# Kernel optimization log

Hardware: AMD Instinct MI355X
Metric: run time of the kernel (lower is better)

Reference implementation:

```python
import jax, jax.numpy as jnp
import numpy as np

MARGIN = 0.3
PD_EPS = 1e-6  # torch.nn.functional.pairwise_distance default eps (added to the diff)


def setup_inputs() -> dict:
    key = jax.random.key(0)
    k1, k2 = jax.random.split(key)
    n, d = 8192, 128
    inputs = jax.random.normal(k1, (n, d), dtype=jnp.float32)
    positive = jax.random.normal(k2, (n, d), dtype=jnp.float32)
    return {"inputs": inputs, "positive": positive}


def reference(inputs, positive):
    # Pairwise squared Euclidean distances: ||xi||^2 + ||xj||^2 - 2 xi.xj  -> [n, n]
    sq = jnp.sum(inputs * inputs, axis=1, keepdims=True)  # [n, 1]
    dist = sq + sq.T - 2.0 * (inputs @ inputs.T)
    dist = jnp.sqrt(jnp.clip(dist, 1e-12, None))

    # Original: dist[i].argsort()[4] -> 5th-nearest (index 0 is self at ~0 distance).
    # Equivalent, avoiding full per-row sort: top-5 smallest distances.
    _, idx = jax.lax.top_k(-dist, 5)  # idx: [n, 5], ascending by distance
    negative = inputs[idx[:, 4]]  # hard negatives, [n, d]

    # TripletMarginLoss(margin=0.3, p=2): pairwise_distance adds eps to the diff.
    d_ap = jnp.linalg.norm(inputs - positive + PD_EPS, axis=1)
    d_an = jnp.linalg.norm(inputs - negative + PD_EPS, axis=1)
    return jnp.mean(jnp.maximum(d_ap - d_an + MARGIN, 0.0))
```

## Files before the change

kernel.cpp:

```cpp
#include <hip/hip_runtime.h>

#define NN 8192
#define DD 128
#define CH 16
#define CPC (NN / CH)
#define TILES (CPC / 64)
#define NPART 64

typedef __bf16 bf16x8 __attribute__((ext_vector_type(8)));
typedef float f32x4 __attribute__((ext_vector_type(4)));

#define PACK_INIT __uint_as_float(0x7F7FFFFFu)

static __device__ __forceinline__ float packsi(float s, unsigned idx) {
  return __uint_as_float((__float_as_uint(s) & 0xFFFFE000u) | idx);
}

#define NET4(S0, S1, S2, S3, v)                                                \
  {                                                                            \
    float v_ = (v), o0 = S0, o1 = S1, o2 = S2;                                 \
    S0 = fminf(o0, v_);                                                        \
    S1 = __builtin_amdgcn_fmed3f(v_, o0, o1);                                  \
    S2 = __builtin_amdgcn_fmed3f(v_, o1, o2);                                  \
    S3 = __builtin_amdgcn_fmed3f(v_, o2, S3);                                  \
  }
#define NET5(S0, S1, S2, S3, S4, v)                                            \
  {                                                                            \
    float v_ = (v), o0 = S0, o1 = S1, o2 = S2, o3 = S3;                        \
    S0 = fminf(o0, v_);                                                        \
    S1 = __builtin_amdgcn_fmed3f(v_, o0, o1);                                  \
    S2 = __builtin_amdgcn_fmed3f(v_, o1, o2);                                  \
    S3 = __builtin_amdgcn_fmed3f(v_, o2, o3);                                  \
    S4 = __builtin_amdgcn_fmed3f(v_, o3, S4);                                  \
  }

static __device__ __forceinline__ unsigned short f2bf(float f) {
  unsigned u = __float_as_uint(f);
  u += 0x7FFFu + ((u >> 16) & 1u);
  return (unsigned short)(u >> 16);
}

__global__ __launch_bounds__(256) void prep_kernel(const float* __restrict__ x,
                                                   unsigned short* __restrict__ xb,
                                                   float* __restrict__ sq,
                                                   float* __restrict__ partial) {
  const int wave = threadIdx.x >> 6, lane = threadIdx.x & 63;
  const int row = blockIdx.x * 4 + wave;
  const float2 v = ((const float2*)(x + (size_t)row * DD))[lane];
  float ss = v.x * v.x + v.y * v.y;
#pragma unroll
  for (int off = 32; off; off >>= 1) ss += __shfl_down(ss, off);
  if (lane == 0) sq[row] = ss;
  unsigned packed = (unsigned)f2bf(v.x) | ((unsigned)f2bf(v.y) << 16);
  ((unsigned*)(xb + (size_t)row * DD))[lane] = packed;
  if (blockIdx.x == 0 && threadIdx.x < NPART) partial[threadIdx.x] = 0.0f;
}

__global__ __launch_bounds__(256, 2) void dist_topk_kernel(
    const unsigned short* __restrict__ xb, const float* __restrict__ sq,
    float* __restrict__ pscore) {
  const int t = threadIdx.x;
  const int wave = t >> 6, lane = t & 63;
  const int lrow = lane & 15, lquad = lane >> 4;
  const int rowBase = blockIdx.x * 256;
  const int chunk = blockIdx.y;
  const int j0 = chunk * CPC;
  const bool hasDiag = ((blockIdx.x >> 1) == (int)blockIdx.y);

  __shared__ unsigned short colsB[2][64 * DD];
  __shared__ float sqs[2][64];

  const int r0 = rowBase + wave * 64 + lrow;
  const unsigned short* ap0 = xb + (size_t)(r0)*DD + lquad * 8;
  const unsigned short* ap1 = xb + (size_t)(r0 + 16) * DD + lquad * 8;
  const unsigned short* ap2 = xb + (size_t)(r0 + 32) * DD + lquad * 8;
  const unsigned short* ap3 = xb + (size_t)(r0 + 48) * DD + lquad * 8;
  bf16x8 a00 = *(const bf16x8*)(ap0), a01 = *(const bf16x8*)(ap0 + 32),
         a02 = *(const bf16x8*)(ap0 + 64), a03 = *(const bf16x8*)(ap0 + 96);
  bf16x8 a10 = *(const bf16x8*)(ap1), a11 = *(const bf16x8*)(ap1 + 32),
         a12 = *(const bf16x8*)(ap1 + 64), a13 = *(const bf16x8*)(ap1 + 96);
  bf16x8 a20 = *(const bf16x8*)(ap2), a21 = *(const bf16x8*)(ap2 + 32),
         a22 = *(const bf16x8*)(ap2 + 64), a23 = *(const bf16x8*)(ap2 + 96);
  bf16x8 a30 = *(const bf16x8*)(ap3), a31 = *(const bf16x8*)(ap3 + 32),
         a32 = *(const bf16x8*)(ap3 + 64), a33 = *(const bf16x8*)(ap3 + 96);

  float q00 = PACK_INIT, q01 = PACK_INIT, q02 = PACK_INIT, q03 = PACK_INIT,
        q04 = PACK_INIT;
  float q10 = PACK_INIT, q11 = PACK_INIT, q12 = PACK_INIT, q13 = PACK_INIT,
        q14 = PACK_INIT;
  float q20 = PACK_INIT, q21 = PACK_INIT, q22 = PACK_INIT, q23 = PACK_INIT,
        q24 = PACK_INIT;
  float q30 = PACK_INIT, q31 = PACK_INIT, q32 = PACK_INIT, q33 = PACK_INIT,
        q34 = PACK_INIT;

  const int sr = t >> 4, sch = t & 15;
  const int dst0 = (sr << 4) | (sch ^ (sr & 15));

  const float4* srcv = (const float4*)(xb + (size_t)j0 * DD);
  float4 g0 = srcv[t], g1 = srcv[t + 256], g2 = srcv[t + 512], g3 = srcv[t + 768];
  float sqv = 0.0f;
  if (t < 64) sqv = sq[j0 + t];

#define KBODY(INSROW)                                                          \
  for (int it = 0; it < TILES; ++it) {                                         \
    const int jt = j0 + it * 64;                                               \
    const int cur = it & 1;                                                    \
    {                                                                          \
      float4* dstv = (float4*)colsB[cur];                                      \
      dstv[dst0] = g0;                                                         \
      dstv[dst0 + 256] = g1;                                                   \
      dstv[dst0 + 512] = g2;                                                   \
      dstv[dst0 + 768] = g3;                                                   \
      if (t < 64) sqs[cur][t] = sqv;                                           \
    }                                                                          \
    if (it + 1 < TILES) {                                                      \
      const float4* nsrc = (const float4*)(xb + (size_t)(jt + 64) * DD);       \
      g0 = nsrc[t]; g1 = nsrc[t + 256]; g2 = nsrc[t + 512]; g3 = nsrc[t + 768];\
      if (t < 64) sqv = sq[jt + 64 + t];                                       \
    }                                                                          \
    __syncthreads();                                                           \
    _Pragma("unroll")                                                          \
    for (int ct = 0; ct < 4; ++ct) {                                           \
      const unsigned short* bb = &colsB[cur][(ct * 16 + lrow) * DD];           \
      bf16x8 b0 = *(const bf16x8*)(bb + (((0 + lquad) ^ lrow) << 3));          \
      bf16x8 b1 = *(const bf16x8*)(bb + (((4 + lquad) ^ lrow) << 3));          \
      bf16x8 b2 = *(const bf16x8*)(bb + (((8 + lquad) ^ lrow) << 3));          \
      bf16x8 b3 = *(const bf16x8*)(bb + (((12 + lquad) ^ lrow) << 3));         \
      f32x4 ac0 = {0.f, 0.f, 0.f, 0.f}, ac1 = {0.f, 0.f, 0.f, 0.f};           \
      f32x4 ac2 = {0.f, 0.f, 0.f, 0.f}, ac3 = {0.f, 0.f, 0.f, 0.f};           \
      ac0 = __builtin_amdgcn_mfma_f32_16x16x32_bf16(b0, a00, ac0, 0, 0, 0);    \
      ac1 = __builtin_amdgcn_mfma_f32_16x16x32_bf16(b0, a10, ac1, 0, 0, 0);    \
      ac2 = __builtin_amdgcn_mfma_f32_16x16x32_bf16(b0, a20, ac2, 0, 0, 0);    \
      ac3 = __builtin_amdgcn_mfma_f32_16x16x32_bf16(b0, a30, ac3, 0, 0, 0);    \
      ac0 = __builtin_amdgcn_mfma_f32_16x16x32_bf16(b1, a01, ac0, 0, 0, 0);    \
      ac1 = __builtin_amdgcn_mfma_f32_16x16x32_bf16(b1, a11, ac1, 0, 0, 0);    \
      ac2 = __builtin_amdgcn_mfma_f32_16x16x32_bf16(b1, a21, ac2, 0, 0, 0);    \
      ac3 = __builtin_amdgcn_mfma_f32_16x16x32_bf16(b1, a31, ac3, 0, 0, 0);    \
      ac0 = __builtin_amdgcn_mfma_f32_16x16x32_bf16(b2, a02, ac0, 0, 0, 0);    \
      ac1 = __builtin_amdgcn_mfma_f32_16x16x32_bf16(b2, a12, ac1, 0, 0, 0);    \
      ac2 = __builtin_amdgcn_mfma_f32_16x16x32_bf16(b2, a22, ac2, 0, 0, 0);    \
      ac3 = __builtin_amdgcn_mfma_f32_16x16x32_bf16(b2, a32, ac3, 0, 0, 0);    \
      ac0 = __builtin_amdgcn_mfma_f32_16x16x32_bf16(b3, a03, ac0, 0, 0, 0);    \
      ac1 = __builtin_amdgcn_mfma_f32_16x16x32_bf16(b3, a13, ac1, 0, 0, 0);    \
      ac2 = __builtin_amdgcn_mfma_f32_16x16x32_bf16(b3, a23, ac2, 0, 0, 0);    \
      ac3 = __builtin_amdgcn_mfma_f32_16x16x32_bf16(b3, a33, ac3, 0, 0, 0);    \
      const f32x4 sq4 = *(const f32x4*)&sqs[cur][ct * 16 + lquad * 4];         \
      const unsigned colb = (unsigned)(jt + ct * 16 + lquad * 4);              \
      _Pragma("unroll")                                                        \
      for (int r = 0; r < 4; ++r) {                                            \
        INSROW(0, packsi(fmaf(-2.0f, ac0[r], sq4[r]), colb + r));              \
        INSROW(1, packsi(fmaf(-2.0f, ac1[r], sq4[r]), colb + r));              \
        INSROW(2, packsi(fmaf(-2.0f, ac2[r], sq4[r]), colb + r));              \
        INSROW(3, packsi(fmaf(-2.0f, ac3[r], sq4[r]), colb + r));              \
      }                                                                        \
    }                                                                          \
  }

#define INS4(G, V) NET4(q##G##0, q##G##1, q##G##2, q##G##3, (V))
#define INS5(G, V) NET5(q##G##0, q##G##1, q##G##2, q##G##3, q##G##4, (V))

  if (hasDiag) {
    KBODY(INS5)
  } else {
    KBODY(INS4)
  }
#undef KBODY

#define MERGE4(G, M)                                                           \
  {                                                                            \
    float o0 = __shfl_xor(q##G##0, M), o1 = __shfl_xor(q##G##1, M),            \
          o2 = __shfl_xor(q##G##2, M), o3 = __shfl_xor(q##G##3, M);            \
    NET4(q##G##0, q##G##1, q##G##2, q##G##3, o0);                              \
    NET4(q##G##0, q##G##1, q##G##2, q##G##3, o1);                              \
    NET4(q##G##0, q##G##1, q##G##2, q##G##3, o2);                              \
    NET4(q##G##0, q##G##1, q##G##2, q##G##3, o3);                              \
  }
#define MERGE5(G, M)                                                           \
  {                                                                            \
    float o0 = __shfl_xor(q##G##0, M), o1 = __shfl_xor(q##G##1, M),            \
          o2 = __shfl_xor(q##G##2, M), o3 = __shfl_xor(q##G##3, M),            \
          o4 = __shfl_xor(q##G##4, M);                                         \
    NET5(q##G##0, q##G##1, q##G##2, q##G##3, q##G##4, o0);                     \
    NET5(q##G##0, q##G##1, q##G##2, q##G##3, q##G##4, o1);                     \
    NET5(q##G##0, q##G##1, q##G##2, q##G##3, q##G##4, o2);                     \
    NET5(q##G##0, q##G##1, q##G##2, q##G##3, q##G##4, o3);                     \
    NET5(q##G##0, q##G##1, q##G##2, q##G##3, q##G##4, o4);                     \
  }
  if (hasDiag) {
    MERGE5(0, 16) MERGE5(1, 16) MERGE5(2, 16) MERGE5(3, 16)
    MERGE5(0, 32) MERGE5(1, 32) MERGE5(2, 32) MERGE5(3, 32)
  } else {
    MERGE4(0, 16) MERGE4(1, 16) MERGE4(2, 16) MERGE4(3, 16)
    MERGE4(0, 32) MERGE4(1, 32) MERGE4(2, 32) MERGE4(3, 32)
  }

  if (lquad == 0) {
    float* b0p = pscore + (size_t)(r0)*80 + chunk * 5;
    b0p[0] = q00; b0p[1] = q01; b0p[2] = q02; b0p[3] = q03; b0p[4] = q04;
    float* b1p = pscore + (size_t)(r0 + 16) * 80 + chunk * 5;
    b1p[0] = q10; b1p[1] = q11; b1p[2] = q12; b1p[3] = q13; b1p[4] = q14;
    float* b2p = pscore + (size_t)(r0 + 32) * 80 + chunk * 5;
    b2p[0] = q20; b2p[1] = q21; b2p[2] = q22; b2p[3] = q23; b2p[4] = q24;
    float* b3p = pscore + (size_t)(r0 + 48) * 80 + chunk * 5;
    b3p[0] = q30; b3p[1] = q31; b3p[2] = q32; b3p[3] = q33; b3p[4] = q34;
  }
}

__global__ __launch_bounds__(256) void final_kernel(const float* __restrict__ x,
                                                    const float* __restrict__ pos,
                                                    const float* __restrict__ pscore,
                                                    float* __restrict__ partial) {
  const int wave = threadIdx.x >> 6, lane = threadIdx.x & 63;
  const int row = blockIdx.x * 4 + wave;

  float q0 = PACK_INIT, q1 = PACK_INIT, q2 = PACK_INIT, q3 = PACK_INIT,
        q4 = PACK_INIT;
  if (lane < CH) {
    const float* b = pscore + (size_t)row * 80 + lane * 5;
    q0 = b[0]; q1 = b[1]; q2 = b[2]; q3 = b[3]; q4 = b[4];
  }
#pragma unroll
  for (int m = 1; m < CH; m <<= 1) {
    float o0 = __shfl_xor(q0, m), o1 = __shfl_xor(q1, m), o2 = __shfl_xor(q2, m),
          o3 = __shfl_xor(q3, m), o4 = __shfl_xor(q4, m);
    NET5(q0, q1, q2, q3, q4, o0);
    NET5(q0, q1, q2, q3, q4, o1);
    NET5(q0, q1, q2, q3, q4, o2);
    NET5(q0, q1, q2, q3, q4, o3);
    NET5(q0, q1, q2, q3, q4, o4);
  }
  const int nidx = (int)(__float_as_uint(__shfl(q4, 0)) & 0x1FFFu);

  const float2 xv  = ((const float2*)(x   + (size_t)row  * DD))[lane];
  const float2 pv  = ((const float2*)(pos + (size_t)row  * DD))[lane];
  const float2 nvv = ((const float2*)(x   + (size_t)nidx * DD))[lane];
  float a0 = xv.x - pv.x + 1e-6f, a1 = xv.y - pv.y + 1e-6f;
  float b0 = xv.x - nvv.x + 1e-6f, b1 = xv.y - nvv.y + 1e-6f;
  float dap = a0 * a0 + a1 * a1;
  float dan = b0 * b0 + b1 * b1;
#pragma unroll
  for (int off = 32; off; off >>= 1) {
    dap += __shfl_down(dap, off);
    dan += __shfl_down(dan, off);
  }
  __shared__ float hs[4];
  if (lane == 0) hs[wave] = fmaxf(sqrtf(dap) - sqrtf(dan) + 0.3f, 0.0f);
  __syncthreads();
  if (threadIdx.x == 0) {
    float s = hs[0] + hs[1] + hs[2] + hs[3];
    atomicAdd(&partial[blockIdx.x & (NPART - 1)], s);
  }
}

__global__ __launch_bounds__(64) void reduce_kernel(const float* __restrict__ partial,
                                                    float* __restrict__ out) {
  float v = partial[threadIdx.x];
#pragma unroll
  for (int off = 32; off; off >>= 1) v += __shfl_down(v, off);
  if (threadIdx.x == 0) out[0] = v * (1.0f / 8192.0f);
}

extern "C" void kernel_launch(void* const* d_in, const int* in_sizes, int n_in,
                              void* d_out, int out_size, void* d_ws, size_t ws_size,
                              hipStream_t stream) {
  const float* x   = (const float*)d_in[0];
  const float* pos = (const float*)d_in[1];
  float* out = (float*)d_out;

  char* w = (char*)d_ws;
  unsigned short* xb = (unsigned short*)w;
  float* sq = (float*)(w + (size_t)NN * DD * 2);
  float* pscore = (float*)(w + (size_t)NN * DD * 2 + (size_t)NN * 4);
  float* partial = (float*)(w + (size_t)NN * DD * 2 + (size_t)NN * 4 +
                            (size_t)NN * 80 * 4);

  prep_kernel<<<NN / 4, 256, 0, stream>>>(x, xb, sq, partial);
  dist_topk_kernel<<<dim3(NN / 256, CH), 256, 0, stream>>>(xb, sq, pscore);
  final_kernel<<<NN / 4, 256, 0, stream>>>(x, pos, pscore, partial);
  reduce_kernel<<<1, 64, 0, stream>>>(partial, out);
}
```

Measured before the change: 109.0 us.

## Fold norm into MFMA accumulator init and stream column tiles via global_load_lds

The per-column norm term is precomputed as -0.5*||x||^2 - 70 and fed in as the MFMA accumulator's initial value. This removes the per-element fmaf from the top-k insertion loop, and the selection flips to a max-network on negated scores. Column tiles are now loaded straight into LDS with global_load_lds instead of passing through registers, and all column norms are staged up front. This cuts VGPR pressure and per-element ALU work. The risk is that the -70 offset, which keeps scores negative so the packed index bits order correctly, may affect precision, and only the single barrier at loop top remains for async-load ordering.

```diff
diff --git a/kernel.cpp b/kernel.cpp
--- a/kernel.cpp
+++ b/kernel.cpp
@@ -10,7 +10,7 @@
 typedef __bf16 bf16x8 __attribute__((ext_vector_type(8)));
 typedef float f32x4 __attribute__((ext_vector_type(4)));
 
-#define PACK_INIT __uint_as_float(0x7F7FFFFFu)
+#define PACK_INIT __uint_as_float(0xFF7FFFFFu)
 
 static __device__ __forceinline__ float packsi(float s, unsigned idx) {
   return __uint_as_float((__float_as_uint(s) & 0xFFFFE000u) | idx);
@@ -19,7 +19,7 @@
 #define NET4(S0, S1, S2, S3, v)                                                \
   {                                                                            \
     float v_ = (v), o0 = S0, o1 = S1, o2 = S2;                                 \
-    S0 = fminf(o0, v_);                                                        \
+    S0 = fmaxf(o0, v_);                                                        \
     S1 = __builtin_amdgcn_fmed3f(v_, o0, o1);                                  \
     S2 = __builtin_amdgcn_fmed3f(v_, o1, o2);                                  \
     S3 = __builtin_amdgcn_fmed3f(v_, o2, S3);                                  \
@@ -27,7 +27,7 @@
 #define NET5(S0, S1, S2, S3, S4, v)                                            \
   {                                                                            \
     float v_ = (v), o0 = S0, o1 = S1, o2 = S2, o3 = S3;                        \
-    S0 = fminf(o0, v_);                                                        \
+    S0 = fmaxf(o0, v_);                                                        \
     S1 = __builtin_amdgcn_fmed3f(v_, o0, o1);                                  \
     S2 = __builtin_amdgcn_fmed3f(v_, o1, o2);                                  \
     S3 = __builtin_amdgcn_fmed3f(v_, o2, o3);                                  \
@@ -38,6 +38,12 @@
   unsigned u = __float_as_uint(f);
   u += 0x7FFFu + ((u >> 16) & 1u);
   return (unsigned short)(u >> 16);
+}
+
+static __device__ __forceinline__ void gload_lds16(const void* g, void* l) {
+  __builtin_amdgcn_global_load_lds(
+      (const __attribute__((address_space(1))) unsigned*)g,
+      (__attribute__((address_space(3))) unsigned*)l, 16, 0, 0);
 }
 
 __global__ __launch_bounds__(256) void prep_kernel(const float* __restrict__ x,
@@ -50,7 +56,7 @@
   float ss = v.x * v.x + v.y * v.y;
 #pragma unroll
   for (int off = 32; off; off >>= 1) ss += __shfl_down(ss, off);
-  if (lane == 0) sq[row] = ss;
+  if (lane == 0) sq[row] = fmaf(-0.5f, ss, -70.0f);
   unsigned packed = (unsigned)f2bf(v.x) | ((unsigned)f2bf(v.y) << 16);
   ((unsigned*)(xb + (size_t)row * DD))[lane] = packed;
   if (blockIdx.x == 0 && threadIdx.x < NPART) partial[threadIdx.x] = 0.0f;
@@ -68,7 +74,7 @@
   const bool hasDiag = ((blockIdx.x >> 1) == (int)blockIdx.y);
 
   __shared__ unsigned short colsB[2][64 * DD];
-  __shared__ float sqs[2][64];
+  __shared__ float sqs_all[CPC];
 
   const int r0 = rowBase + wave * 64 + lrow;
   const unsigned short* ap0 = xb + (size_t)(r0)*DD + lquad * 8;
@@ -93,32 +99,28 @@
   float q30 = PACK_INIT, q31 = PACK_INIT, q32 = PACK_INIT, q33 = PACK_INIT,
         q34 = PACK_INIT;
 
-  const int sr = t >> 4, sch = t & 15;
-  const int dst0 = (sr << 4) | (sch ^ (sr & 15));
-
-  const float4* srcv = (const float4*)(xb + (size_t)j0 * DD);
-  float4 g0 = srcv[t], g1 = srcv[t + 256], g2 = srcv[t + 512], g3 = srcv[t + 768];
-  float sqv = 0.0f;
-  if (t < 64) sqv = sq[j0 + t];
+  const int psl = (t & ~15) | ((t ^ (t >> 4)) & 15);
+
+#define ISSUE_TILE(buf, jtrow)                                                 \
+  {                                                                            \
+    const float4* s_ = (const float4*)(xb + (size_t)(jtrow)*DD);               \
+    char* l_ = (char*)(&colsB[buf][0]) + wave * 1024;                          \
+    gload_lds16(s_ + psl, l_);                                                 \
+    gload_lds16(s_ + psl + 256, l_ + 4096);                                    \
+    gload_lds16(s_ + psl + 512, l_ + 8192);                                    \
+    gload_lds16(s_ + psl + 768, l_ + 12288);                                   \
+  }
+
+  sqs_all[t] = sq[j0 + t];
+  sqs_all[t + 256] = sq[j0 + 256 + t];
+  ISSUE_TILE(0, j0)
 
 #define KBODY(INSROW)                                                          \
   for (int it = 0; it < TILES; ++it) {                                         \
     const int jt = j0 + it * 64;                                               \
     const int cur = it & 1;                                                    \
-    {                                                                          \
-      float4* dstv = (float4*)colsB[cur];                                      \
-      dstv[dst0] = g0;                                                         \
-      dstv[dst0 + 256] = g1;                                                   \
-      dstv[dst0 + 512] = g2;                                                   \
-      dstv[dst0 + 768] = g3;                                                   \
-      if (t < 64) sqs[cur][t] = sqv;                                           \
-    }                                                                          \
-    if (it + 1 < TILES) {                                                      \
-      const float4* nsrc = (const float4*)(xb + (size_t)(jt + 64) * DD);       \
-      g0 = nsrc[t]; g1 = nsrc[t + 256]; g2 = nsrc[t + 512]; g3 = nsrc[t + 768];\
-      if (t < 64) sqv = sq[jt + 64 + t];                                       \
-    }                                                                          \
-    __syncthreads();                                                           \
+    __syncthreads();          \
+    if (it + 1 < TILES) { ISSUE_TILE(cur ^ 1, jt + 64) }                       \
     _Pragma("unroll")                                                          \
     for (int ct = 0; ct < 4; ++ct) {                                           \
       const unsigned short* bb = &colsB[cur][(ct * 16 + lrow) * DD];           \
@@ -126,12 +128,11 @@
       bf16x8 b1 = *(const bf16x8*)(bb + (((4 + lquad) ^ lrow) << 3));          \
       bf16x8 b2 = *(const bf16x8*)(bb + (((8 + lquad) ^ lrow) << 3));          \
       bf16x8 b3 = *(const bf16x8*)(bb + (((12 + lquad) ^ lrow) << 3));         \
-      f32x4 ac0 = {0.f, 0.f, 0.f, 0.f}, ac1 = {0.f, 0.f, 0.f, 0.f};           \
-      f32x4 ac2 = {0.f, 0.f, 0.f, 0.f}, ac3 = {0.f, 0.f, 0.f, 0.f};           \
-      ac0 = __builtin_amdgcn_mfma_f32_16x16x32_bf16(b0, a00, ac0, 0, 0, 0);    \
-      ac1 = __builtin_amdgcn_mfma_f32_16x16x32_bf16(b0, a10, ac1, 0, 0, 0);    \
-      ac2 = __builtin_amdgcn_mfma_f32_16x16x32_bf16(b0, a20, ac2, 0, 0, 0);    \
-      ac3 = __builtin_amdgcn_mfma_f32_16x16x32_bf16(b0, a30, ac3, 0, 0, 0);    \
+      const f32x4 nsq4 = *(const f32x4*)&sqs_all[it * 64 + ct * 16 + lquad * 4];\
+      f32x4 ac0 = __builtin_amdgcn_mfma_f32_16x16x32_bf16(b0, a00, nsq4, 0, 0, 0);\
+      f32x4 ac1 = __builtin_amdgcn_mfma_f32_16x16x32_bf16(b0, a10, nsq4, 0, 0, 0);\
+      f32x4 ac2 = __builtin_amdgcn_mfma_f32_16x16x32_bf16(b0, a20, nsq4, 0, 0, 0);\
+      f32x4 ac3 = __builtin_amdgcn_mfma_f32_16x16x32_bf16(b0, a30, nsq4, 0, 0, 0);\
       ac0 = __builtin_amdgcn_mfma_f32_16x16x32_bf16(b1, a01, ac0, 0, 0, 0);    \
       ac1 = __builtin_amdgcn_mfma_f32_16x16x32_bf16(b1, a11, ac1, 0, 0, 0);    \
       ac2 = __builtin_amdgcn_mfma_f32_16x16x32_bf16(b1, a21, ac2, 0, 0, 0);    \
@@ -144,14 +145,14 @@
       ac1 = __builtin_amdgcn_mfma_f32_16x16x32_bf16(b3, a13, ac1, 0, 0, 0);    \
       ac2 = __builtin_amdgcn_mfma_f32_16x16x32_bf16(b3, a23, ac2, 0, 0, 0);    \
       ac3 = __builtin_amdgcn_mfma_f32_16x16x32_bf16(b3, a33, ac3, 0, 0, 0);    \
-      const f32x4 sq4 = *(const f32x4*)&sqs[cur][ct * 16 + lquad * 4];         \
       const unsigned colb = (unsigned)(jt + ct * 16 + lquad * 4);              \
       _Pragma("unroll")                                                        \
       for (int r = 0; r < 4; ++r) {                                            \
-        INSROW(0, packsi(fmaf(-2.0f, ac0[r], sq4[r]), colb + r));              \
-        INSROW(1, packsi(fmaf(-2.0f, ac1[r], sq4[r]), colb + r));              \
-        INSROW(2, packsi(fmaf(-2.0f, ac2[r], sq4[r]), colb + r));              \
-        INSROW(3, packsi(fmaf(-2.0f, ac3[r], sq4[r]), colb + r));              \
+        const unsigned cr = colb + r;                                          \
+        INSROW(0, packsi(ac0[r], cr));                                         \
+        INSROW(1, packsi(ac1[r], cr));                                         \
+        INSROW(2, packsi(ac2[r], cr));                                         \
+        INSROW(3, packsi(ac3[r], cr));                                         \
       }                                                                        \
     }                                                                          \
   }
```

Measured after the change: 103.9 us. -4.7%, faster.
